# Performance work log

Hardware: AMD Instinct MI355X
Metric: run time of the kernel (lower is better)

## Reference

```python
import jax, jax.numpy as jnp
import numpy as np

# Constants mirroring MS / MultiLayers_MS forward args (scalars closed over)
HEADS = 8
BETA = 0.5          # GAT_MS_2_3 init arg 'beta' (mean-shift coordinate gate strength)
T = 1.0             # temperature 't' forward arg
BAND_WIDTH = 1.0    # 'band_width' forward arg
MAX_ITER = 3        # 'max_iter' forward arg (iterative mean-shift steps)
SELF_DISTANCE = 0.01  # 'self_distance' forward arg: distance assigned to the diagonal
USE_STD_ATT = False # 'use_std_att' forward arg
NEG_INF = -1e9


def setup_inputs() -> dict:
    key = jax.random.key(0)
    ks = jax.random.split(key, 16)
    N, D = 3072, 256
    x = jax.random.normal(ks[0], (N, D), dtype=jnp.float32)
    xyz = jax.random.normal(ks[1], (N, 3), dtype=jnp.float32) * 3.0
    # delta_y = |y_hat - y_hat^T| as produced by GAT_Classifier (detached)
    y_hat = jax.random.uniform(ks[2], (N, 1), dtype=jnp.float32)
    delta_y = jnp.abs(y_hat - y_hat.T)
    distance_mask = jax.random.uniform(ks[3], (N, N)) < 0.3   # sparse pairwise gate
    big_inter_mask = jax.random.uniform(ks[4], (N, N)) < 0.9  # inter-chain gate
    s = 1.0 / np.sqrt(D)  # ~ xavier_uniform scale for D x D
    def lin_w(k):
        return jax.random.uniform(k, (D, D), jnp.float32, minval=-s, maxval=s)
    Wq, Wk, Wv, Wo = lin_w(ks[5]), lin_w(ks[6]), lin_w(ks[7]), lin_w(ks[8])
    z = jnp.zeros((D,), jnp.float32)
    return dict(x=x, xyz=xyz, delta_y=delta_y,
                distance_mask=distance_mask, big_inter_mask=big_inter_mask,
                Wq=Wq, bq=z, Wk=Wk, bk=z, Wv=Wv, bv=z, Wo=Wo, bo=z)


def _mean_shift(xyz, q, k, v, delta_y, valid):
    """Iterative distance/band-masked multi-head attention (mean_shift).
    q,k,v: [N,H,Dh]; delta_y: [N,N]; valid: [N,N] bool. Returns (xyz, feat [N,D])."""
    N, H, Dh = q.shape
    eye = jnp.eye(N, dtype=bool)
    # content scores, computed once (q,k fixed across iterations)
    scores = jnp.einsum('nhd,mhd->hnm', q, k) / jnp.sqrt(jnp.float32(Dh))  # [H,N,N]
    if USE_STD_ATT:
        mu = scores.mean(axis=-1, keepdims=True)
        sd = scores.std(axis=-1, keepdims=True)
        scores = (scores - mu) / (sd + 1e-5)
    inv2bw2 = 1.0 / (2.0 * BAND_WIDTH * BAND_WIDTH)
    feat = None
    for _ in range(MAX_ITER):
        # pairwise squared distances of current coordinates [N,N]
        d2 = jnp.sum((xyz[:, None, :] - xyz[None, :, :]) ** 2, axis=-1)
        d2 = jnp.where(eye, SELF_DISTANCE ** 2, d2)
        # banded logits: content score, Gaussian distance band, prediction-difference gate
        logits = T * scores - BETA * (d2 * inv2bw2) - delta_y  # [H,N,N]
        logits = jnp.where(valid, logits, NEG_INF)
        attn = jax.nn.softmax(logits, axis=-1)                 # [H,N,N]
        xyz = attn.mean(axis=0) @ xyz                          # mean-shift coords [N,3]
        feat = jnp.einsum('hnm,mhd->nhd', attn, v).reshape(N, H * Dh)
    return xyz, feat


def reference(x, xyz, delta_y, distance_mask, big_inter_mask,
              Wq, bq, Wk, bk, Wv, bv, Wo, bo):
    N, D = x.shape
    H, Dh = HEADS, D // HEADS
    q = (x @ Wq + bq).reshape(N, H, Dh)
    k = (x @ Wk + bk).reshape(N, H, Dh)
    v = (x @ Wv + bv).reshape(N, H, Dh)
    eye = jnp.eye(N, dtype=bool)
    valid = (distance_mask & big_inter_mask) | eye  # keep self to avoid empty rows
    xyz_out, feat = _mean_shift(xyz, q, k, v, delta_y, valid)
    out = feat @ Wo + bo + x   # out_proj + residual (MS.forward)
    return xyz_out, out
```

## Files before the change

kernel.cpp:

```cpp
#include <hip/hip_runtime.h>
#include <hip/hip_fp16.h>

#define NN 3072
#define DD 256
#define NH 8
#define SPLIT 4
#define KT (NN / SPLIT / 64)
#define NKT2 (NN / 64)
#define VHALF ((NN / 16) * 256)
#define LN2INV 1.4426950408889634f

typedef _Float16 h16;
typedef __attribute__((ext_vector_type(4))) _Float16 half4;
typedef __attribute__((ext_vector_type(8))) _Float16 half8;
typedef __attribute__((ext_vector_type(4))) float f32x4;

#if __has_builtin(__builtin_amdgcn_exp2f)
#define EXP2(x) __builtin_amdgcn_exp2f(x)
#else
#define EXP2(x) __expf((x) * 0.69314718056f)
#endif

#define MFMA16(a, b, c) __builtin_amdgcn_mfma_f32_16x16x16f16(a, b, c, 0, 0, 0)

__device__ __forceinline__ void async16(const h16* g, h16* l, int lane) {
#if __has_builtin(__builtin_amdgcn_global_load_lds)
  __builtin_amdgcn_global_load_lds(
      (const __attribute__((address_space(1))) void*)(g + (size_t)lane * 8),
      (__attribute__((address_space(3))) void*)l, 16, 0, 0);
#else
  *(half8*)(l + lane * 8) = *(const half8*)(g + (size_t)lane * 8);
#endif
}

__device__ inline void write_aug(int q, float x, float y, float z,
                                 h16* __restrict__ qaug, h16* __restrict__ kaug,
                                 h16* __restrict__ xzT3) {
  float sx = 0.5f * LN2INV * x, sy = 0.5f * LN2INV * y, sz = 0.5f * LN2INV * z;
  h16 shx = (h16)sx, shy = (h16)sy, shz = (h16)sz;
  h16 slx = (h16)(sx - (float)shx), sly = (h16)(sy - (float)shy), slz = (h16)(sz - (float)shz);
  h16 hx = (h16)x, hy = (h16)y, hz = (h16)z;
  h16 lx = (h16)(x - (float)hx), ly = (h16)(y - (float)hy), lz = (h16)(z - (float)hz);
  float n2n = -0.25f * LN2INV * (x * x + y * y + z * z);
  h16 nh = (h16)n2n, nl = (h16)(n2n - (float)nh);
  h16 qa[16], ka[16];
  #pragma unroll
  for (int i = 0; i < 16; ++i) { qa[i] = (h16)0.f; ka[i] = (h16)0.f; }
  qa[0] = shx; qa[1] = shy; qa[2] = shz;
  qa[3] = shx; qa[4] = shy; qa[5] = shz;
  qa[6] = slx; qa[7] = sly; qa[8] = slz;
  qa[9] = (h16)1.f; qa[10] = (h16)1.f;
  qa[11] = (h16)n2n;
  ka[0] = hx; ka[1] = hy; ka[2] = hz;
  ka[3] = lx; ka[4] = ly; ka[5] = lz;
  ka[6] = hx; ka[7] = hy; ka[8] = hz;
  ka[9] = nh; ka[10] = nl;
  ka[11] = (h16)1.f;
  *(half8*)(qaug + (size_t)q * 16) = ((half8*)qa)[0];
  *(half8*)(qaug + (size_t)q * 16 + 8) = ((half8*)qa)[1];
  *(half8*)(kaug + (size_t)q * 16) = ((half8*)ka)[0];
  *(half8*)(kaug + (size_t)q * 16 + 8) = ((half8*)ka)[1];
  int kt2 = q >> 6, kk = q & 63;
  int f = kk >> 4, qd = (kk >> 2) & 3, j = kk & 3;
  h16* b = xzT3 + ((size_t)kt2 << 10) + f * 256 + qd * 64 + j;
  b[0] = (h16)1.f;
  b[4] = hx; b[8] = hy; b[12] = hz;
  b[16] = lx; b[20] = ly; b[24] = lz;
  #pragma unroll
  for (int m = 7; m < 16; ++m) b[m * 4] = (h16)0.f;
}

__global__ __launch_bounds__(256) void k_convert(
    const float* __restrict__ x, const float* __restrict__ xyz,
    h16* __restrict__ xb, h16* __restrict__ qaug,
    h16* __restrict__ kaug, h16* __restrict__ xzT3) {
  int t = blockIdx.x * 256 + threadIdx.x;
  const int NX = NN * DD;
  if (t < NX) { xb[t] = (h16)x[t]; return; }
  int q = t - NX;
  if (q < NN) write_aug(q, xyz[q * 3], xyz[q * 3 + 1], xyz[q * 3 + 2], qaug, kaug, xzT3);
}

__global__ __launch_bounds__(256) void k_wt(
    const float* __restrict__ Wq, const float* __restrict__ Wk,
    const float* __restrict__ Wv, const float* __restrict__ Wo,
    h16* __restrict__ wtq, h16* __restrict__ wtk, h16* __restrict__ wtv,
    h16* __restrict__ wto) {
  __shared__ float tile[32][33];
  int m = blockIdx.z;
  const float* W = (m == 0) ? Wq : (m == 1) ? Wk : (m == 2) ? Wv : Wo;
  h16* wt = (m == 0) ? wtq : (m == 1) ? wtk : (m == 2) ? wtv : wto;
  int n0 = blockIdx.x * 32, k0 = blockIdx.y * 32;
  int tx = threadIdx.x & 31, ty = threadIdx.x >> 5;
  #pragma unroll
  for (int i = 0; i < 4; ++i)
    tile[ty + i * 8][tx] = W[(size_t)(k0 + ty + i * 8) * 256 + n0 + tx];
  __syncthreads();
  #pragma unroll
  for (int i = 0; i < 4; ++i)
    wt[(size_t)(n0 + ty + i * 8) * 256 + k0 + tx] = (h16)tile[tx][ty + i * 8];
}

__global__ __launch_bounds__(256) void k_prep(
    const float* __restrict__ dy, const int* __restrict__ dm,
    const int* __restrict__ bim, h16* __restrict__ dynT3) {
  __shared__ h16 sv[16][1036];
  int qt = blockIdx.y;
  int cb = blockIdx.x;
  int t = threadIdx.x;
  int c0 = cb * 1024 + t * 4;
  #pragma unroll
  for (int r = 0; r < 16; ++r) {
    int row = qt * 16 + r;
    size_t idx = (size_t)row * NN + c0;
    int4 m4 = *(const int4*)(dm + idx);
    int4 b4 = *(const int4*)(bim + idx);
    float4 d4 = *(const float4*)(dy + idx);
    h16* s = &sv[r][t * 4];
    int mm[4] = {m4.x & b4.x, m4.y & b4.y, m4.z & b4.z, m4.w & b4.w};
    float dd[4] = {d4.x, d4.y, d4.z, d4.w};
    #pragma unroll
    for (int j = 0; j < 4; ++j) {
      bool diag = (row == c0 + j);
      bool valid = (mm[j] != 0) | diag;
      s[j] = (h16)(valid ? (-LN2INV * (dd[j] + (diag ? 2.5e-5f : 0.f))) : -43281.f);
    }
  }
  __syncthreads();
  #pragma unroll
  for (int s2 = 0; s2 < 8; ++s2) {
    int s = t + s2 * 256;
    int tile = s >> 7;
    int sl = s & 127;
    int chunk = sl >> 6;
    int lane = sl & 63;
    int row = lane & 15, quad = lane >> 4;
    int base = tile * 64 + chunk * 32 + quad * 4;
    half4 lo = *(const half4*)&sv[row][base];
    half4 hi = *(const half4*)&sv[row][base + 16];
    half8 o;
    #pragma unroll
    for (int j = 0; j < 4; ++j) { o[j] = lo[j]; o[j + 4] = hi[j]; }
    h16* dst = dynT3 + (((size_t)qt * NKT2 + (cb * 16 + tile)) << 10) + sl * 8;
    *(half8*)dst = o;
  }
}

__device__ inline void gemm_body(const h16* __restrict__ A, const h16* __restrict__ Bt,
                                 const float* __restrict__ bias, void* __restrict__ out,
                                 const float* __restrict__ resid, int M, int mode,
                                 float scale, int bx, int by) {
  int lane = threadIdx.x & 63;
  int wave = threadIdx.x >> 6;
  int col = lane & 15, quad = lane >> 4;
  int m0 = bx * 32;
  int n0 = by * 64 + wave * 16;
  f32x4 acc[2];
  acc[0] = (f32x4){0.f, 0.f, 0.f, 0.f};
  acc[1] = (f32x4){0.f, 0.f, 0.f, 0.f};
  #pragma unroll
  for (int kk = 0; kk < DD; kk += 32) {
    half8 b = *(const half8*)(Bt + (size_t)(n0 + col) * DD + kk + quad * 8);
    #pragma unroll
    for (int mr = 0; mr < 2; ++mr) {
      half8 a = *(const half8*)(A + (size_t)(m0 + mr * 16 + col) * DD + kk + quad * 8);
      acc[mr] = __builtin_amdgcn_mfma_f32_16x16x32_f16(a, b, acc[mr], 0, 0, 0);
    }
  }
  float bb = bias[n0 + col];
  #pragma unroll
  for (int mr = 0; mr < 2; ++mr) {
    #pragma unroll
    for (int r = 0; r < 4; ++r) {
      int m = m0 + mr * 16 + quad * 4 + r;
      int n = n0 + col;
      float v = acc[mr][r] + bb;
      if (mode == 0)      ((h16*)out)[(size_t)m * DD + n] = (h16)(v * scale);
      else if (mode == 3) ((h16*)out)[((size_t)(n >> 5) * NN + m) * 32 + (n & 31)] = (h16)v;
      else if (mode == 4) {
        int hh = n >> 5, d = n & 31;
        size_t a = ((((size_t)hh * 2 + (d >> 4)) * (NN / 16) + (m >> 4)) * 64 +
                    ((m >> 2) & 3) * 16 + (d & 15)) * 4 + (m & 3);
        ((h16*)out)[a] = (h16)v;
      }
      else ((float*)out)[(size_t)m * DD + n] = v + resid[(size_t)m * DD + n];
    }
  }
}

__global__ __launch_bounds__(256) void k_gemm(
    const h16* __restrict__ A, const h16* __restrict__ Bt,
    const float* __restrict__ bias, void* __restrict__ out,
    const float* __restrict__ resid, int M, int mode, float scale) {
  gemm_body(A, Bt, bias, out, resid, M, mode, scale, blockIdx.x, blockIdx.y);
}

__global__ __launch_bounds__(256) void k_gemm3(
    const h16* __restrict__ A, const h16* __restrict__ wtq,
    const h16* __restrict__ wtk, const h16* __restrict__ wtv,
    const float* __restrict__ bq, const float* __restrict__ bk,
    const float* __restrict__ bv, h16* __restrict__ qb, h16* __restrict__ kbh,
    h16* __restrict__ vA, float qscale) {
  int z = blockIdx.z;
  const h16* Bt = (z == 0) ? wtq : (z == 1) ? wtk : wtv;
  const float* bias = (z == 0) ? bq : (z == 1) ? bk : bv;
  void* out = (z == 0) ? (void*)qb : (z == 1) ? (void*)kbh : (void*)vA;
  int mode = (z == 0) ? 0 : (z == 1) ? 3 : 4;
  gemm_body(A, Bt, bias, out, nullptr, NN, mode, (z == 0) ? qscale : 1.f,
            blockIdx.x, blockIdx.y);
}

__device__ __forceinline__ void stage_tile(int h, int lane, int qt, int kt2,
                                           const h16* __restrict__ dynT3,
                                           const h16* __restrict__ kaug,
                                           const h16* __restrict__ xzT3,
                                           h16* bdy, h16* bka, h16* bxz) {
  if (h < 2)
    async16(dynT3 + (((size_t)qt * NKT2 + kt2) << 10) + h * 512, bdy + h * 512, lane);
  else if (h < 4)
    async16(kaug + ((size_t)kt2 << 10) + (h - 2) * 512, bka + (h - 2) * 512, lane);
  else if (h < 6)
    async16(xzT3 + ((size_t)kt2 << 10) + (h - 4) * 512, bxz + (h - 4) * 512, lane);
}

__device__ __forceinline__ void ldkf(const h16* __restrict__ kbh_h, int k0,
                                     int col, int quad, half8 kf[4]) {
  #pragma unroll
  for (int f = 0; f < 4; ++f)
    kf[f] = *(const half8*)(kbh_h + (size_t)(k0 + f * 16 + col) * 32 + quad * 8);
}

template <int LAST>
__device__ __forceinline__ void ms_compute(
    const h16* __restrict__ bdy, const h16* __restrict__ bka,
    const h16* __restrict__ bxz, const half8 kf[4], half8 qaf, half8 qf,
    const h16* __restrict__ vA0, int lane, int col, int quad,
    f32x4& accS, f32x4& fc0, f32x4& fc1) {
  half8 kz = {};
  half8 dv0 = *(const half8*)(bdy + lane * 8);
  half8 dv1 = *(const half8*)(bdy + 512 + lane * 8);
  #pragma unroll
  for (int f = 0; f < 4; ++f) {
    half8 ka = (quad < 2) ? *(const half8*)(bka + (f * 16 + col) * 16 + quad * 8) : kz;
    half8 dv = (f & 2) ? dv1 : dv0;
    f32x4 cc;
    #pragma unroll
    for (int r = 0; r < 4; ++r) cc[r] = (float)dv[(f & 1) * 4 + r];
    f32x4 g = __builtin_amdgcn_mfma_f32_16x16x32_f16(ka, qaf, cc, 0, 0, 0);
    f32x4 s = __builtin_amdgcn_mfma_f32_16x16x32_f16(kf[f], qf, g, 0, 0, 0);
    half4 pv;
    #pragma unroll
    for (int r = 0; r < 4; ++r) pv[r] = (h16)EXP2(s[r]);
    half4 xa = *(const half4*)(bxz + f * 256 + lane * 4);
    accS = MFMA16(xa, pv, accS);
    if (LAST) {
      half4 v0 = *(const half4*)(vA0 + f * 256 + lane * 4);
      half4 v1 = *(const half4*)(vA0 + VHALF + f * 256 + lane * 4);
      fc0 = MFMA16(v0, pv, fc0);
      fc1 = MFMA16(v1, pv, fc1);
    }
  }
}

template <int LAST>
__global__ __launch_bounds__(512, 4) void k_msattn(
    const h16* __restrict__ qb, const h16* __restrict__ kbh,
    const h16* __restrict__ vA, const h16* __restrict__ dynT3,
    const h16* __restrict__ qaug, const h16* __restrict__ kaug,
    const h16* __restrict__ xzT3, float* __restrict__ den_s,
    float* __restrict__ axh_s, float* __restrict__ axl_s,
    float* __restrict__ numT) {
  __shared__ h16 s_dy[2][1024];
  __shared__ h16 s_ka[2][1024];
  __shared__ h16 s_xz[2][1024];
  const int tid = threadIdx.x;
  const int h = tid >> 6;
  const int lane = tid & 63;
  const int col = lane & 15;
  const int quad = lane >> 4;
  const int qt = blockIdx.x;
  const int q0 = qt * 16;
  const int tb = blockIdx.y * KT;

  half8 kz = {};
  half8 qf = *(const half8*)(qb + (size_t)(q0 + col) * DD + h * 32 + quad * 8);
  half8 qaf = (quad < 2) ? *(const half8*)(qaug + (size_t)(q0 + col) * 16 + quad * 8) : kz;
  const h16* kbh_h = kbh + (size_t)h * NN * 32;
  const h16* vb = vA + (size_t)h * 2 * (NN / 16) * 256;
  f32x4 accS = (f32x4){0.f, 0.f, 0.f, 0.f};
  f32x4 fc0 = (f32x4){0.f, 0.f, 0.f, 0.f};
  f32x4 fc1 = (f32x4){0.f, 0.f, 0.f, 0.f};
  half8 kfA[4], kfB[4];

  stage_tile(h, lane, qt, tb, dynT3, kaug, xzT3, s_dy[0], s_ka[0], s_xz[0]);
  ldkf(kbh_h, tb * 64, col, quad, kfA);
  __syncthreads();
  #pragma unroll 1
  for (int kt = 0; kt < KT; kt += 2) {
    int t1 = tb + kt + 1;
    stage_tile(h, lane, qt, t1, dynT3, kaug, xzT3, s_dy[1], s_ka[1], s_xz[1]);
    ldkf(kbh_h, t1 * 64, col, quad, kfB);
    ms_compute<LAST>(s_dy[0], s_ka[0], s_xz[0], kfA, qaf, qf,
                     vb + (size_t)(tb + kt) * 1024,
                     lane, col, quad, accS, fc0, fc1);
    __syncthreads();
    int t2 = (kt + 2 < KT) ? tb + kt + 2 : t1;
    if (kt + 2 < KT)
      stage_tile(h, lane, qt, t2, dynT3, kaug, xzT3, s_dy[0], s_ka[0], s_xz[0]);
    ldkf(kbh_h, t2 * 64, col, quad, kfA);
    ms_compute<LAST>(s_dy[1], s_ka[1], s_xz[1], kfB, qaf, qf,
                     vb + (size_t)t1 * 1024,
                     lane, col, quad, accS, fc0, fc1);
    __syncthreads();
  }

  int q = q0 + col;
  size_t sidx = (size_t)(blockIdx.y * NH + h) * NN + q;
  if (quad == 0) {
    den_s[sidx] = accS[0];
    axh_s[sidx * 3 + 0] = accS[1];
    axh_s[sidx * 3 + 1] = accS[2];
    axh_s[sidx * 3 + 2] = accS[3];
  } else if (quad == 1) {
    axl_s[sidx * 3 + 0] = accS[0];
    axl_s[sidx * 3 + 1] = accS[1];
    axl_s[sidx * 3 + 2] = accS[2];
  }
  if (LAST) {
    #pragma unroll
    for (int r = 0; r < 4; ++r) {
      atomicAdd(&numT[(size_t)(h * 32 + quad * 4 + r) * NN + q], fc0[r]);
      atomicAdd(&numT[(size_t)(h * 32 + 16 + quad * 4 + r) * NN + q], fc1[r]);
    }
  }
}

__global__ __launch_bounds__(256) void k_combine(
    const float* __restrict__ den_s, const float* __restrict__ axh_s,
    const float* __restrict__ axl_s, float* __restrict__ den_tot,
    h16* __restrict__ qaug, h16* __restrict__ kaug, h16* __restrict__ xzT3,
    float* __restrict__ out3) {
  int q = blockIdx.x * 256 + threadIdx.x;
  if (q >= NN) return;
  float X = 0.f, Y = 0.f, Z = 0.f;
  #pragma unroll
  for (int h = 0; h < NH; ++h) {
    float d = 0.f, x = 0.f, y = 0.f, z = 0.f;
    #pragma unroll
    for (int s = 0; s < SPLIT; ++s) {
      size_t idx = (size_t)(s * NH + h) * NN + q;
      d += den_s[idx];
      x += axh_s[idx * 3 + 0] + axl_s[idx * 3 + 0];
      y += axh_s[idx * 3 + 1] + axl_s[idx * 3 + 1];
      z += axh_s[idx * 3 + 2] + axl_s[idx * 3 + 2];
    }
    den_tot[h * NN + q] = d;
    float inv = 0.125f / d;
    X = fmaf(x, inv, X);
    Y = fmaf(y, inv, Y);
    Z = fmaf(z, inv, Z);
  }
  if (out3) {
    out3[q * 3 + 0] = X;
    out3[q * 3 + 1] = Y;
    out3[q * 3 + 2] = Z;
  } else {
    write_aug(q, X, Y, Z, qaug, kaug, xzT3);
  }
}

__global__ __launch_bounds__(256) void k_finish(
    const float* __restrict__ numT, const float* __restrict__ den_tot,
    h16* __restrict__ featb) {
  __shared__ float tile[32][33];
  int q0 = blockIdx.x * 32, d0 = blockIdx.y * 32;
  int tx = threadIdx.x & 31, ty = threadIdx.x >> 5;
  #pragma unroll
  for (int i = 0; i < 4; ++i)
    tile[ty + i * 8][tx] = numT[(size_t)(d0 + ty + i * 8) * NN + q0 + tx];
  __syncthreads();
  int h = d0 >> 5;
  #pragma unroll
  for (int i = 0; i < 4; ++i) {
    int q = q0 + ty + i * 8;
    float inv = 1.f / den_tot[h * NN + q];
    featb[(size_t)q * DD + d0 + tx] = (h16)(tile[tx][ty + i * 8] * inv);
  }
}

extern "C" void kernel_launch(void* const* d_in, const int* in_sizes, int n_in,
                              void* d_out, int out_size, void* d_ws, size_t ws_size,
                              hipStream_t stream) {
  const float* x   = (const float*)d_in[0];
  const float* xyz = (const float*)d_in[1];
  const float* dy  = (const float*)d_in[2];
  const int* dm    = (const int*)d_in[3];
  const int* bim   = (const int*)d_in[4];
  const float* Wq = (const float*)d_in[5];
  const float* bq = (const float*)d_in[6];
  const float* Wk = (const float*)d_in[7];
  const float* bk = (const float*)d_in[8];
  const float* Wv = (const float*)d_in[9];
  const float* bv = (const float*)d_in[10];
  const float* Wo = (const float*)d_in[11];
  const float* bo = (const float*)d_in[12];

  char* p = (char*)d_ws;
  h16* xb  = (h16*)p; p += (size_t)NN * DD * 2;
  h16* wtq = (h16*)p; p += 256 * 256 * 2;
  h16* wtk = (h16*)p; p += 256 * 256 * 2;
  h16* wtv = (h16*)p; p += 256 * 256 * 2;
  h16* wto = (h16*)p; p += 256 * 256 * 2;
  h16* qb    = (h16*)p; p += (size_t)NN * DD * 2;
  h16* kbh   = (h16*)p; p += (size_t)NN * DD * 2;
  h16* vA    = (h16*)p; p += (size_t)NN * DD * 2;
  h16* featb = (h16*)p; p += (size_t)NN * DD * 2;
  h16* dynT3 = (h16*)p; p += (size_t)NN * NN * 2;
  h16* qaug  = (h16*)p; p += (size_t)NN * 16 * 2;
  h16* kaug  = (h16*)p; p += (size_t)NN * 16 * 2;
  h16* xzT3  = (h16*)p; p += (size_t)NKT2 * 1024 * 2;
  float* den_s = (float*)p; p += (size_t)SPLIT * NH * NN * 4;
  float* axh_s = (float*)p; p += (size_t)SPLIT * NH * NN * 3 * 4;
  float* axl_s = (float*)p; p += (size_t)SPLIT * NH * NN * 3 * 4;
  float* den_tot = (float*)p; p += (size_t)NH * NN * 4;
  float* numT = (float*)p; p += (size_t)DD * NN * 4;

  hipMemsetAsync(numT, 0, (size_t)DD * NN * 4, stream);
  k_convert<<<(NN * DD + NN + 255) / 256, 256, 0, stream>>>(x, xyz, xb, qaug,
                                                            kaug, xzT3);
  k_wt<<<dim3(8, 8, 4), 256, 0, stream>>>(Wq, Wk, Wv, Wo, wtq, wtk, wtv, wto);
  k_prep<<<dim3(3, 192), 256, 0, stream>>>(dy, dm, bim, dynT3);
  k_gemm3<<<dim3(96, 4, 3), 256, 0, stream>>>(xb, wtq, wtk, wtv, bq, bk, bv,
                                              qb, kbh, vA,
                                              0.17677669529663689f * LN2INV);

  float* xyz_final = (float*)d_out;
  float* out_final = (float*)d_out + NN * 3;

  k_msattn<0><<<dim3(NN / 16, SPLIT), 512, 0, stream>>>(
      qb, kbh, vA, dynT3, qaug, kaug, xzT3, den_s, axh_s, axl_s, nullptr);
  k_combine<<<12, 256, 0, stream>>>(den_s, axh_s, axl_s, den_tot,
                                    qaug, kaug, xzT3, nullptr);
  k_msattn<0><<<dim3(NN / 16, SPLIT), 512, 0, stream>>>(
      qb, kbh, vA, dynT3, qaug, kaug, xzT3, den_s, axh_s, axl_s, nullptr);
  k_combine<<<12, 256, 0, stream>>>(den_s, axh_s, axl_s, den_tot,
                                    qaug, kaug, xzT3, nullptr);
  k_msattn<1><<<dim3(NN / 16, SPLIT), 512, 0, stream>>>(
      qb, kbh, vA, dynT3, qaug, kaug, xzT3, den_s, axh_s, axl_s, numT);
  k_combine<<<12, 256, 0, stream>>>(den_s, axh_s, axl_s, den_tot,
                                    nullptr, nullptr, nullptr, xyz_final);
  k_finish<<<dim3(96, 8), 256, 0, stream>>>(numT, den_tot, featb);
  k_gemm<<<dim3(96, 4), 256, 0, stream>>>(featb, wto, bo, out_final, x, NN, 2, 1.f);
}
```

Baseline: 373.3 us.

## Fuse numT zeroing into convert, parallelize combine over heads, hoist xz loads

Zeroing of the numT accumulator moves from a separate memset into the k_convert kernel, saving one launch. k_combine now assigns one thread per (query, head) and reduces across the 8 heads with xor shuffles, launching 96 blocks instead of 12 so more CUs share the work. In the attention inner loop, the xyz-augmented fragments are loaded before the MFMA chain and the wave priority is raised around it. The combine rewrite adds shuffle traffic, and the hoisted loads increase register pressure in the attention kernel.

Result: faster. 324.9 us (-12.9%).

```diff
diff --git a/kernel.cpp b/kernel.cpp
--- a/kernel.cpp
+++ b/kernel.cpp
@@ -73,10 +73,11 @@
 __global__ __launch_bounds__(256) void k_convert(
     const float* __restrict__ x, const float* __restrict__ xyz,
     h16* __restrict__ xb, h16* __restrict__ qaug,
-    h16* __restrict__ kaug, h16* __restrict__ xzT3) {
+    h16* __restrict__ kaug, h16* __restrict__ xzT3,
+    float* __restrict__ numT) {
   int t = blockIdx.x * 256 + threadIdx.x;
   const int NX = NN * DD;
-  if (t < NX) { xb[t] = (h16)x[t]; return; }
+  if (t < NX) { xb[t] = (h16)x[t]; numT[t] = 0.f; return; }
   int q = t - NX;
   if (q < NN) write_aug(q, xyz[q * 3], xyz[q * 3 + 1], xyz[q * 3 + 2], qaug, kaug, xzT3);
 }
@@ -239,6 +240,11 @@
   half8 kz = {};
   half8 dv0 = *(const half8*)(bdy + lane * 8);
   half8 dv1 = *(const half8*)(bdy + 512 + lane * 8);
+  half4 xa[4];
+  #pragma unroll
+  for (int f = 0; f < 4; ++f)
+    xa[f] = *(const half4*)(bxz + f * 256 + lane * 4);
+  __builtin_amdgcn_s_setprio(1);
   #pragma unroll
   for (int f = 0; f < 4; ++f) {
     half8 ka = (quad < 2) ? *(const half8*)(bka + (f * 16 + col) * 16 + quad * 8) : kz;
@@ -251,8 +257,7 @@
     half4 pv;
     #pragma unroll
     for (int r = 0; r < 4; ++r) pv[r] = (h16)EXP2(s[r]);
-    half4 xa = *(const half4*)(bxz + f * 256 + lane * 4);
-    accS = MFMA16(xa, pv, accS);
+    accS = MFMA16(xa[f], pv, accS);
     if (LAST) {
       half4 v0 = *(const half4*)(vA0 + f * 256 + lane * 4);
       half4 v1 = *(const half4*)(vA0 + VHALF + f * 256 + lane * 4);
@@ -260,6 +265,7 @@
       fc1 = MFMA16(v1, pv, fc1);
     }
   }
+  __builtin_amdgcn_s_setprio(0);
 }
 
 template <int LAST>
@@ -340,32 +346,34 @@
     const float* __restrict__ axl_s, float* __restrict__ den_tot,
     h16* __restrict__ qaug, h16* __restrict__ kaug, h16* __restrict__ xzT3,
     float* __restrict__ out3) {
-  int q = blockIdx.x * 256 + threadIdx.x;
-  if (q >= NN) return;
-  float X = 0.f, Y = 0.f, Z = 0.f;
-  #pragma unroll
-  for (int h = 0; h < NH; ++h) {
-    float d = 0.f, x = 0.f, y = 0.f, z = 0.f;
-    #pragma unroll
-    for (int s = 0; s < SPLIT; ++s) {
-      size_t idx = (size_t)(s * NH + h) * NN + q;
-      d += den_s[idx];
-      x += axh_s[idx * 3 + 0] + axl_s[idx * 3 + 0];
-      y += axh_s[idx * 3 + 1] + axl_s[idx * 3 + 1];
-      z += axh_s[idx * 3 + 2] + axl_s[idx * 3 + 2];
-    }
-    den_tot[h * NN + q] = d;
-    float inv = 0.125f / d;
-    X = fmaf(x, inv, X);
-    Y = fmaf(y, inv, Y);
-    Z = fmaf(z, inv, Z);
-  }
-  if (out3) {
-    out3[q * 3 + 0] = X;
-    out3[q * 3 + 1] = Y;
-    out3[q * 3 + 2] = Z;
-  } else {
-    write_aug(q, X, Y, Z, qaug, kaug, xzT3);
+  int h = threadIdx.x & 7;
+  int q = blockIdx.x * 32 + (threadIdx.x >> 3);
+  float d = 0.f, x = 0.f, y = 0.f, z = 0.f;
+  #pragma unroll
+  for (int s = 0; s < SPLIT; ++s) {
+    size_t idx = (size_t)(s * NH + h) * NN + q;
+    d += den_s[idx];
+    x += axh_s[idx * 3 + 0] + axl_s[idx * 3 + 0];
+    y += axh_s[idx * 3 + 1] + axl_s[idx * 3 + 1];
+    z += axh_s[idx * 3 + 2] + axl_s[idx * 3 + 2];
+  }
+  den_tot[h * NN + q] = d;
+  float inv = 0.125f / d;
+  float X = x * inv, Y = y * inv, Z = z * inv;
+  #pragma unroll
+  for (int m = 1; m < 8; m <<= 1) {
+    X += __shfl_xor(X, m);
+    Y += __shfl_xor(Y, m);
+    Z += __shfl_xor(Z, m);
+  }
+  if (h == 0) {
+    if (out3) {
+      out3[q * 3 + 0] = X;
+      out3[q * 3 + 1] = Y;
+      out3[q * 3 + 2] = Z;
+    } else {
+      write_aug(q, X, Y, Z, qaug, kaug, xzT3);
+    }
   }
 }
 
@@ -425,9 +433,8 @@
   float* den_tot = (float*)p; p += (size_t)NH * NN * 4;
   float* numT = (float*)p; p += (size_t)DD * NN * 4;
 
-  hipMemsetAsync(numT, 0, (size_t)DD * NN * 4, stream);
   k_convert<<<(NN * DD + NN + 255) / 256, 256, 0, stream>>>(x, xyz, xb, qaug,
-                                                            kaug, xzT3);
+                                                            kaug, xzT3, numT);
   k_wt<<<dim3(8, 8, 4), 256, 0, stream>>>(Wq, Wk, Wv, Wo, wtq, wtk, wtv, wto);
   k_prep<<<dim3(3, 192), 256, 0, stream>>>(dy, dm, bim, dynT3);
   k_gemm3<<<dim3(96, 4, 3), 256, 0, stream>>>(xb, wtq, wtk, wtv, bq, bk, bv,
@@ -439,15 +446,15 @@
 
   k_msattn<0><<<dim3(NN / 16, SPLIT), 512, 0, stream>>>(
       qb, kbh, vA, dynT3, qaug, kaug, xzT3, den_s, axh_s, axl_s, nullptr);
-  k_combine<<<12, 256, 0, stream>>>(den_s, axh_s, axl_s, den_tot,
+  k_combine<<<96, 256, 0, stream>>>(den_s, axh_s, axl_s, den_tot,
                                     qaug, kaug, xzT3, nullptr);
   k_msattn<0><<<dim3(NN / 16, SPLIT), 512, 0, stream>>>(
       qb, kbh, vA, dynT3, qaug, kaug, xzT3, den_s, axh_s, axl_s, nullptr);
-  k_combine<<<12, 256, 0, stream>>>(den_s, axh_s, axl_s, den_tot,
+  k_combine<<<96, 256, 0, stream>>>(den_s, axh_s, axl_s, den_tot,
                                     qaug, kaug, xzT3, nullptr);
   k_msattn<1><<<dim3(NN / 16, SPLIT), 512, 0, stream>>>(
       qb, kbh, vA, dynT3, qaug, kaug, xzT3, den_s, axh_s, axl_s, numT);
-  k_combine<<<12, 256, 0, stream>>>(den_s, axh_s, axl_s, den_tot,
+  k_combine<<<96, 256, 0, stream>>>(den_s, axh_s, axl_s, den_tot,
                                     nullptr, nullptr, nullptr, xyz_final);
   k_finish<<<dim3(96, 8), 256, 0, stream>>>(numT, den_tot, featb);
   k_gemm<<<dim3(96, 4), 256, 0, stream>>>(featb, wto, bo, out_final, x, NN, 2, 1.f);
```
